# Kernel tuning notes

Hardware: AMD Instinct MI355X
Metric: run time of the kernel (lower is better)

## Reference

```python
import jax, jax.numpy as jnp
import numpy as np

N = 50000
HEADS1, HIM = 8, 16
NEG_SLOPE = 0.2


def gat_conv(x, src, dst, W, a_src, a_dst, bias, heads, out_dim, concat):
    n = x.shape[0]
    h = (x @ W).reshape(n, heads, out_dim)                      # [N,H,D]
    al_src = jnp.einsum('nhd,hd->nh', h, a_src)                  # [N,H]
    al_dst = jnp.einsum('nhd,hd->nh', h, a_dst)                  # [N,H]
    e = jax.nn.leaky_relu(al_src[src] + al_dst[dst], NEG_SLOPE)  # [E,H]
    # segment softmax over incoming edges of each destination node
    e_max = jax.ops.segment_max(e, dst, num_segments=n)
    e_max = jnp.where(jnp.isfinite(e_max), e_max, 0.0)
    ex = jnp.exp(e - e_max[dst])
    denom = jax.ops.segment_sum(ex, dst, num_segments=n)
    denom = jnp.where(denom == 0.0, 1.0, denom)
    alpha = ex / denom[dst]                                      # [E,H]
    msg = h[src] * alpha[:, :, None]                             # [E,H,D]
    out = jax.ops.segment_sum(msg, dst, num_segments=n)          # [N,H,D]
    out = out.reshape(n, heads * out_dim) if concat else out.mean(axis=1)
    return out + bias


def setup_inputs() -> dict:
    key = jax.random.key(0)
    ks = jax.random.split(key, 12)
    num_feature, out_feature, him = 128, 121, HIM
    E = 800000
    x = jax.random.normal(ks[0], (N, num_feature), dtype=jnp.float32)
    edge_index = jax.random.randint(ks[1], (2, E), 0, N, dtype=jnp.int64)
    s = 0.1
    W1 = jax.random.normal(ks[2], (num_feature, HEADS1 * him), dtype=jnp.float32) * s
    a_src1 = jax.random.normal(ks[3], (HEADS1, him), dtype=jnp.float32) * s
    a_dst1 = jax.random.normal(ks[4], (HEADS1, him), dtype=jnp.float32) * s
    b1 = jnp.zeros((HEADS1 * him,), dtype=jnp.float32)
    W2 = jax.random.normal(ks[5], (HEADS1 * him, out_feature), dtype=jnp.float32) * s
    a_src2 = jax.random.normal(ks[6], (1, out_feature), dtype=jnp.float32) * s
    a_dst2 = jax.random.normal(ks[7], (1, out_feature), dtype=jnp.float32) * s
    b2 = jnp.zeros((out_feature,), dtype=jnp.float32)
    return {"x": x, "edge_index": edge_index, "W1": W1, "a_src1": a_src1,
            "a_dst1": a_dst1, "b1": b1, "W2": W2, "a_src2": a_src2,
            "a_dst2": a_dst2, "b2": b2}


def reference(x, edge_index, W1, a_src1, a_dst1, b1, W2, a_src2, a_dst2, b2):
    n = x.shape[0]
    loops = jnp.arange(n, dtype=edge_index.dtype)
    src = jnp.concatenate([edge_index[0], loops])  # add self-loops (PyG default)
    dst = jnp.concatenate([edge_index[1], loops])
    h = gat_conv(x, src, dst, W1, a_src1, a_dst1, b1, HEADS1, HIM, True)
    h = jax.nn.relu(h)
    out = gat_conv(h, src, dst, W2, a_src2, a_dst2, b2, 1, W2.shape[1], True)
    return out
```

## Files before the change

kernel.cpp:

```cpp
#include <hip/hip_runtime.h>
#include <hip/hip_fp16.h>

#define NEG_SLOPE 0.2f

typedef __fp16 half8v __attribute__((ext_vector_type(8)));
typedef float f32x4 __attribute__((ext_vector_type(4)));
typedef unsigned uint4u __attribute__((ext_vector_type(4), aligned(4)));
typedef float f32x4u __attribute__((ext_vector_type(4), aligned(4)));

__device__ __forceinline__ float lrelu(float x) {
    return fmaxf(x, 0.0f) + NEG_SLOPE * fminf(x, 0.0f);
}

__device__ __forceinline__ unsigned fkey(float f) {
    unsigned u = __float_as_uint(f);
    return (u & 0x80000000u) ? ~u : (u | 0x80000000u);
}
__device__ __forceinline__ float funkey(unsigned k) {
    return __uint_as_float((k & 0x80000000u) ? (k & 0x7fffffffu) : ~k);
}


__global__ __launch_bounds__(256) void scan_reduce(const int* __restrict__ cnt,
                                                   int* __restrict__ bsum, int n) {
    __shared__ int sm[256];
    int base = blockIdx.x * 1024 + threadIdx.x * 4;
    int s = 0;
#pragma unroll
    for (int j = 0; j < 4; ++j) {
        int i = base + j;
        if (i < n) s += cnt[i];
    }
    sm[threadIdx.x] = s;
    __syncthreads();
#pragma unroll
    for (int off = 128; off >= 1; off >>= 1) {
        if (threadIdx.x < off) sm[threadIdx.x] += sm[threadIdx.x + off];
        __syncthreads();
    }
    if (threadIdx.x == 0) bsum[blockIdx.x] = sm[0];
}

__global__ __launch_bounds__(256) void scan_bsum256(int* __restrict__ bsum, int nb) {
    __shared__ int sm[256];
    int v = (threadIdx.x < (unsigned)nb) ? bsum[threadIdx.x] : 0;
    sm[threadIdx.x] = v;
    __syncthreads();
    for (int off = 1; off < 256; off <<= 1) {
        int y = (threadIdx.x >= off) ? sm[threadIdx.x - off] : 0;
        __syncthreads();
        sm[threadIdx.x] += y;
        __syncthreads();
    }
    if (threadIdx.x < (unsigned)nb) bsum[threadIdx.x] = sm[threadIdx.x] - v;
}

__global__ __launch_bounds__(256) void scan_write(const int* __restrict__ cnt,
                                                  const int* __restrict__ bsum,
                                                  int* __restrict__ rp, int n) {
    __shared__ int sm[256];
    int base = blockIdx.x * 1024 + threadIdx.x * 4;
    int v[4];
    int s = 0;
#pragma unroll
    for (int j = 0; j < 4; ++j) {
        int i = base + j;
        v[j] = (i < n) ? cnt[i] : 0;
        s += v[j];
    }
    sm[threadIdx.x] = s;
    __syncthreads();
#pragma unroll
    for (int off = 1; off < 256; off <<= 1) {
        int y = (threadIdx.x >= off) ? sm[threadIdx.x - off] : 0;
        __syncthreads();
        sm[threadIdx.x] += y;
        __syncthreads();
    }
    int run = sm[threadIdx.x] - s + bsum[blockIdx.x];
#pragma unroll
    for (int j = 0; j < 4; ++j) {
        int i = base + j;
        if (i < n) {
            rp[i] = run;
            run += v[j];
            if (i == n - 1) rp[n] = run;
        }
    }
}


__global__ __launch_bounds__(256) void rhist1_kernel(const int* __restrict__ dst,
                                                     int* __restrict__ h, int E, int nblk) {
    __shared__ int lh[256];
    lh[threadIdx.x] = 0;
    __syncthreads();
    int base = blockIdx.x * 1024;
#pragma unroll
    for (int j = 0; j < 4; ++j) {
        int i = base + j * 256 + threadIdx.x;
        if (i < E) atomicAdd(&lh[dst[i] & 255], 1);
    }
    __syncthreads();
    h[threadIdx.x * nblk + blockIdx.x] = lh[threadIdx.x];
}

__global__ __launch_bounds__(256) void rhist2_kernel(const unsigned* __restrict__ kv,
                                                     int* __restrict__ h, int E, int nblk) {
    __shared__ int lh[256];
    lh[threadIdx.x] = 0;
    __syncthreads();
    int base = blockIdx.x * 1024;
#pragma unroll
    for (int j = 0; j < 4; ++j) {
        int i = base + j * 256 + threadIdx.x;
        if (i < E) atomicAdd(&lh[kv[i] >> 24], 1);
    }
    __syncthreads();
    h[threadIdx.x * nblk + blockIdx.x] = lh[threadIdx.x];
}

template <int SH, bool PACK>
__global__ __launch_bounds__(256) void rscat_kernel(const unsigned* __restrict__ in,
                                                    const int* __restrict__ srcp,
                                                    const int* __restrict__ dstp,
                                                    unsigned* __restrict__ outv,
                                                    const int* __restrict__ scanned,
                                                    int E, int nblk) {
    __shared__ unsigned items[1024];
    __shared__ unsigned sorted[1024];
    __shared__ int lh[256], lstart[256], rbase[256];
    __shared__ int wcnt[4][256];

    int tid = threadIdx.x, blk = blockIdx.x;
    int base = blk * 1024;
    int k = min(1024, E - base);
    lh[tid] = 0;
    rbase[tid] = 0;
#pragma unroll
    for (int j = 0; j < 4; ++j) {
        int idx = j * 256 + tid;
        unsigned v = 0u;
        if (base + idx < E) {
            if constexpr (PACK)
                v = ((unsigned)dstp[base + idx] << 16) | (unsigned)srcp[base + idx];
            else
                v = in[base + idx];
        }
        items[idx] = v;
    }
    __syncthreads();
#pragma unroll
    for (int j = 0; j < 4; ++j) {
        int idx = j * 256 + tid;
        if (idx < k) atomicAdd(&lh[(items[idx] >> SH) & 255], 1);
    }
    __syncthreads();
    int sv = lh[tid];
    lstart[tid] = sv;
    __syncthreads();
    for (int off = 1; off < 256; off <<= 1) {
        int y = (tid >= off) ? lstart[tid - off] : 0;
        __syncthreads();
        lstart[tid] += y;
        __syncthreads();
    }
    int excl = lstart[tid] - sv;
    __syncthreads();
    lstart[tid] = excl;
    __syncthreads();

    int lane = tid & 63, wave = tid >> 6;
#pragma unroll
    for (int it = 0; it < 4; ++it) {
        int idx = it * 256 + tid;
        unsigned v = items[idx];
        int d = (v >> SH) & 255;
        bool valid = idx < k;
        unsigned long long m = __ballot(valid);
#pragma unroll
        for (int b = 0; b < 8; ++b) {
            unsigned long long bb = __ballot((d >> b) & 1);
            m &= ((d >> b) & 1) ? bb : ~bb;
        }
        int lanerank = __popcll(m & ((1ull << lane) - 1ull));
        int wtot = __popcll(m);
        wcnt[0][tid] = 0; wcnt[1][tid] = 0; wcnt[2][tid] = 0; wcnt[3][tid] = 0;
        __syncthreads();
        if (valid && lanerank == 0) wcnt[wave][d] = wtot;
        __syncthreads();
        if (valid) {
            int cw = 0;
            for (int w = 0; w < wave; ++w) cw += wcnt[w][d];
            sorted[lstart[d] + rbase[d] + cw + lanerank] = v;
        }
        __syncthreads();
        rbase[tid] += wcnt[0][tid] + wcnt[1][tid] + wcnt[2][tid] + wcnt[3][tid];
        __syncthreads();
    }
#pragma unroll
    for (int j = 0; j < 4; ++j) {
        int i = j * 256 + tid;
        if (i < k) {
            unsigned v = sorted[i];
            int d = (v >> SH) & 255;
            outv[scanned[d * nblk + blk] + (i - lstart[d])] = v;
        }
    }
}


__global__ void rp_kernel(const unsigned* __restrict__ kv, int* __restrict__ rp,
                          int E, int N) {
    int i = blockIdx.x * 256 + threadIdx.x;
    if (i >= E) return;
    int cur = (int)(kv[i] >> 16);
    int prev = (i == 0) ? -1 : (int)(kv[i - 1] >> 16);
    for (int t = prev + 1; t <= cur; ++t) rp[t] = i;
    if (i == E - 1)
        for (int t = cur + 1; t <= N; ++t) rp[t] = E;
}


template <int H>
__global__ __launch_bounds__(256) void gmax_kernel(const float* __restrict__ a,
                                                   unsigned* __restrict__ gm, int total) {
    __shared__ unsigned sm[256];
    unsigned loc = 0;
    int stride = 256 * gridDim.x;
    for (int i = blockIdx.x * 256 + threadIdx.x; i < total; i += stride)
        loc = max(loc, fkey(a[i]));
    sm[threadIdx.x] = loc;
    __syncthreads();
    for (int off = 128; off >= H; off >>= 1) {
        if (threadIdx.x < off) sm[threadIdx.x] = max(sm[threadIdx.x], sm[threadIdx.x + off]);
        __syncthreads();
    }
    if (threadIdx.x < H) atomicMax(&gm[threadIdx.x], sm[threadIdx.x]);
}


__global__ __launch_bounds__(256) void w1_kernel(const unsigned* __restrict__ kv,
                                                 const float* __restrict__ alS,
                                                 const float* __restrict__ alD,
                                                 const unsigned* __restrict__ gm,
                                                 float* __restrict__ w1t, int E) {
    int e = blockIdx.x * 256 + threadIdx.x;
    if (e >= E) return;
    unsigned k = kv[e];
    int s = (int)(k & 0xFFFFu), t = (int)(k >> 16);
    float sv[8], dv[8];
    *(f32x4*)&sv[0] = *(const f32x4*)(alS + (size_t)s * 8);
    *(f32x4*)&sv[4] = *(const f32x4*)(alS + (size_t)s * 8 + 4);
    *(f32x4*)&dv[0] = *(const f32x4*)(alD + (size_t)t * 8);
    *(f32x4*)&dv[4] = *(const f32x4*)(alD + (size_t)t * 8 + 4);
#pragma unroll
    for (int h = 0; h < 8; ++h) {
        float m = lrelu(funkey(gm[h]) + dv[h]);
        w1t[(size_t)h * E + e] = __expf(lrelu(sv[h] + dv[h]) - m);
    }
}

__global__ void w2_kernel(const unsigned* __restrict__ kv, const float* __restrict__ alS,
                          const float* __restrict__ alD, const unsigned* __restrict__ gm,
                          float* __restrict__ w2v, int E) {
    int e = blockIdx.x * 256 + threadIdx.x;
    if (e >= E) return;
    unsigned k = kv[e];
    int s = (int)(k & 0xFFFFu), t = (int)(k >> 16);
    float adT = alD[t];
    w2v[e] = __expf(lrelu(alS[s] + adT) - lrelu(funkey(gm[0]) + adT));
}


template <int NC, typename AT>
__global__ __launch_bounds__(256) void gemm_mfma(const AT* __restrict__ A,
                                                 const float* __restrict__ B,
                                                 __half* __restrict__ C, int M) {
    __shared__ __half Bt[128][136];

    {
        int t = threadIdx.x;
        int c = t & 127;
        int kq = t >> 7;
#pragma unroll
        for (int ch = 0; ch < 8; ++ch) {
            int k0 = kq * 64 + ch * 8;
            half8v hv;
#pragma unroll
            for (int j = 0; j < 8; ++j) {
                float v = (c < NC) ? B[(size_t)(k0 + j) * NC + c] : 0.0f;
                hv[j] = (__fp16)v;
            }
            *(half8v*)&Bt[c][k0] = hv;
        }
    }
    __syncthreads();

    const int wid = threadIdx.x >> 6;
    const int lane = threadIdx.x & 63;
    const int li = lane & 15;
    const int lg = lane >> 4;

    int row = blockIdx.x * 64 + wid * 16 + li;
    int rowc = min(row, M - 1);

    half8v a[4];
#pragma unroll
    for (int ks = 0; ks < 4; ++ks) {
        int q = ks * 4 + lg;
        if constexpr (sizeof(AT) == 2) {
            a[ks] = *((const half8v*)(A + (size_t)rowc * 128) + q);
        } else {
            const float4* p = (const float4*)(A + (size_t)rowc * 128) + 2 * q;
            float4 a0 = p[0], a1 = p[1];
            half8v hv;
            hv[0] = (__fp16)a0.x; hv[1] = (__fp16)a0.y; hv[2] = (__fp16)a0.z; hv[3] = (__fp16)a0.w;
            hv[4] = (__fp16)a1.x; hv[5] = (__fp16)a1.y; hv[6] = (__fp16)a1.z; hv[7] = (__fp16)a1.w;
            a[ks] = hv;
        }
    }

    f32x4 acc[8];
#pragma unroll
    for (int ct = 0; ct < 8; ++ct) acc[ct] = (f32x4)0.0f;

#pragma unroll
    for (int ks = 0; ks < 4; ++ks) {
#pragma unroll
        for (int ct = 0; ct < 8; ++ct) {
            half8v b = *(const half8v*)&Bt[ct * 16 + li][ks * 32 + 8 * lg];
            acc[ct] = __builtin_amdgcn_mfma_f32_16x16x32_f16(a[ks], b, acc[ct], 0, 0, 0);
        }
    }

    int orow = blockIdx.x * 64 + wid * 16 + 4 * lg;
#pragma unroll
    for (int ct = 0; ct < 8; ++ct) {
#pragma unroll
        for (int r = 0; r < 4; ++r) {
            int rr = orow + r;
            if (rr < M) C[(size_t)rr * 128 + ct * 16 + li] = __float2half(acc[ct][r]);
        }
    }
}


__global__ void al1_kernel(const __half* __restrict__ h1h, const float* __restrict__ as,
                           const float* __restrict__ ad, float* __restrict__ alS,
                           float* __restrict__ alD, int N) {
    int g = blockIdx.x * 256 + threadIdx.x;
    if (g >= N * 8) return;
    int r = g >> 3, h = g & 7;
    const __half2* hp = (const __half2*)(h1h + (size_t)r * 128 + h * 16);
    const float* sp = as + h * 16;
    const float* dp = ad + h * 16;
    float s = 0.f, d = 0.f;
#pragma unroll
    for (int q = 0; q < 8; ++q) {
        float2 v = __half22float2(hp[q]);
        s = fmaf(v.x, sp[2 * q], s);
        d = fmaf(v.x, dp[2 * q], d);
        s = fmaf(v.y, sp[2 * q + 1], s);
        d = fmaf(v.y, dp[2 * q + 1], d);
    }
    alS[g] = s;
    alD[g] = d;
}

__global__ __launch_bounds__(256) void al2_kernel(const __half* __restrict__ h3h,
                                                  const float* __restrict__ as,
                                                  const float* __restrict__ ad,
                                                  float* __restrict__ alS,
                                                  float* __restrict__ alD, int N, int NC) {
    int lane = threadIdx.x & 63;
    int r = blockIdx.x * 4 + (threadIdx.x >> 6);
    if (r >= N) return;
    float s = 0.f, d = 0.f;
    for (int c = lane; c < NC; c += 64) {
        float v = __half2float(h3h[(size_t)r * 128 + c]);
        s = fmaf(v, as[c], s);
        d = fmaf(v, ad[c], d);
    }
#pragma unroll
    for (int off = 32; off; off >>= 1) {
        s += __shfl_down(s, off);
        d += __shfl_down(d, off);
    }
    if (lane == 0) { alS[r] = s; alD[r] = d; }
}


__global__ __launch_bounds__(256) void agg1_kernel(
    const __half* __restrict__ h1h, const float* __restrict__ alS,
    const float* __restrict__ alD, const float* __restrict__ b1,
    const int* __restrict__ rp, const unsigned* __restrict__ kv,
    const float* __restrict__ w1t, const unsigned* __restrict__ gm,
    __half* __restrict__ h2h, int N, int E) {
    int t = blockIdx.x * 4 + (threadIdx.x >> 6);
    int lane = threadIdx.x & 63;
    int h = lane >> 3;

    float adh = alD[t * 8 + h];
    float mh = lrelu(funkey(gm[h]) + adh);
    int e0 = rp[t], e1 = rp[t + 1];

    float ex = __expf(lrelu(alS[t * 8 + h] + adh) - mh);
    float dsum = ex, dsum2 = 0.f;
    float2 hs = __half22float2(*(const __half2*)(h1h + (size_t)t * 128 + 2 * lane));
    float fx = ex * hs.x, fy = ex * hs.y;
    const float* wrow = w1t + (size_t)h * E;

    int e = e0;
    for (; e + 16 <= e1; e += 16) {
        uint4u kk[4];
        f32x4u ww[4];
#pragma unroll
        for (int q = 0; q < 4; ++q) {
            kk[q] = *(const uint4u*)&kv[e + 4 * q];
            ww[q] = *(const f32x4u*)&wrow[e + 4 * q];
        }
        float2 ff[16];
#pragma unroll
        for (int q = 0; q < 4; ++q)
#pragma unroll
            for (int r = 0; r < 4; ++r)
                ff[q * 4 + r] = __half22float2(
                    *(const __half2*)(h1h + (size_t)(kk[q][r] & 0xFFFFu) * 128 + 2 * lane));
#pragma unroll
        for (int q = 0; q < 4; ++q) {
            if (q & 1) dsum2 += (ww[q][0] + ww[q][1]) + (ww[q][2] + ww[q][3]);
            else       dsum  += (ww[q][0] + ww[q][1]) + (ww[q][2] + ww[q][3]);
#pragma unroll
            for (int r = 0; r < 4; ++r) {
                float w = ww[q][r];
                float2 f = ff[q * 4 + r];
                fx = fmaf(w, f.x, fx);
                fy = fmaf(w, f.y, fy);
            }
        }
    }
    if (e + 8 <= e1) {
        uint4u ka = *(const uint4u*)&kv[e];
        uint4u kb = *(const uint4u*)&kv[e + 4];
        f32x4u wa = *(const f32x4u*)&wrow[e];
        f32x4u wb = *(const f32x4u*)&wrow[e + 4];
        float2 f0 = __half22float2(*(const __half2*)(h1h + (size_t)(ka.x & 0xFFFFu) * 128 + 2 * lane));
        float2 f1 = __half22float2(*(const __half2*)(h1h + (size_t)(ka.y & 0xFFFFu) * 128 + 2 * lane));
        float2 f2 = __half22float2(*(const __half2*)(h1h + (size_t)(ka.z & 0xFFFFu) * 128 + 2 * lane));
        float2 f3 = __half22float2(*(const __half2*)(h1h + (size_t)(ka.w & 0xFFFFu) * 128 + 2 * lane));
        float2 f4 = __half22float2(*(const __half2*)(h1h + (size_t)(kb.x & 0xFFFFu) * 128 + 2 * lane));
        float2 f5 = __half22float2(*(const __half2*)(h1h + (size_t)(kb.y & 0xFFFFu) * 128 + 2 * lane));
        float2 f6 = __half22float2(*(const __half2*)(h1h + (size_t)(kb.z & 0xFFFFu) * 128 + 2 * lane));
        float2 f7 = __half22float2(*(const __half2*)(h1h + (size_t)(kb.w & 0xFFFFu) * 128 + 2 * lane));
        dsum += (wa[0] + wa[1]) + (wa[2] + wa[3]);
        dsum2 += (wb[0] + wb[1]) + (wb[2] + wb[3]);
        fx = fmaf(wa[0], f0.x, fx); fy = fmaf(wa[0], f0.y, fy);
        fx = fmaf(wa[1], f1.x, fx); fy = fmaf(wa[1], f1.y, fy);
        fx = fmaf(wa[2], f2.x, fx); fy = fmaf(wa[2], f2.y, fy);
        fx = fmaf(wa[3], f3.x, fx); fy = fmaf(wa[3], f3.y, fy);
        fx = fmaf(wb[0], f4.x, fx); fy = fmaf(wb[0], f4.y, fy);
        fx = fmaf(wb[1], f5.x, fx); fy = fmaf(wb[1], f5.y, fy);
        fx = fmaf(wb[2], f6.x, fx); fy = fmaf(wb[2], f6.y, fy);
        fx = fmaf(wb[3], f7.x, fx); fy = fmaf(wb[3], f7.y, fy);
        e += 8;
    }
    if (e + 4 <= e1) {
        uint4u ka = *(const uint4u*)&kv[e];
        f32x4u wa = *(const f32x4u*)&wrow[e];
        float2 f0 = __half22float2(*(const __half2*)(h1h + (size_t)(ka.x & 0xFFFFu) * 128 + 2 * lane));
        float2 f1 = __half22float2(*(const __half2*)(h1h + (size_t)(ka.y & 0xFFFFu) * 128 + 2 * lane));
        float2 f2 = __half22float2(*(const __half2*)(h1h + (size_t)(ka.z & 0xFFFFu) * 128 + 2 * lane));
        float2 f3 = __half22float2(*(const __half2*)(h1h + (size_t)(ka.w & 0xFFFFu) * 128 + 2 * lane));
        dsum += (wa[0] + wa[1]) + (wa[2] + wa[3]);
        fx = fmaf(wa[0], f0.x, fx); fy = fmaf(wa[0], f0.y, fy);
        fx = fmaf(wa[1], f1.x, fx); fy = fmaf(wa[1], f1.y, fy);
        fx = fmaf(wa[2], f2.x, fx); fy = fmaf(wa[2], f2.y, fy);
        fx = fmaf(wa[3], f3.x, fx); fy = fmaf(wa[3], f3.y, fy);
        e += 4;
    }
    for (; e < e1; ++e) {
        int s0 = (int)(kv[e] & 0xFFFFu);
        float w0 = wrow[e];
        float2 f0 = __half22float2(*(const __half2*)(h1h + (size_t)s0 * 128 + 2 * lane));
        dsum2 += w0;
        fx = fmaf(w0, f0.x, fx); fy = fmaf(w0, f0.y, fy);
    }
    dsum += dsum2;
    float inv = 1.0f / dsum;
    float2 bb = *(const float2*)(b1 + 2 * lane);
    float ox = fmaxf(fmaf(fx, inv, bb.x), 0.0f);
    float oy = fmaxf(fmaf(fy, inv, bb.y), 0.0f);
    *(__half2*)(h2h + (size_t)t * 128 + 2 * lane) = __floats2half2_rn(ox, oy);
}


__global__ __launch_bounds__(256) void agg2_kernel(
    const __half* __restrict__ h3h, const float* __restrict__ alS,
    const float* __restrict__ alD, const float* __restrict__ b2,
    const int* __restrict__ rp, const unsigned* __restrict__ kv,
    const float* __restrict__ w2v, const unsigned* __restrict__ gm,
    float* __restrict__ out, int N, int NC) {
    int t = blockIdx.x * 4 + (threadIdx.x >> 6);
    int lane = threadIdx.x & 63;

    float adT = alD[t];
    float m = lrelu(funkey(gm[0]) + adT);
    int e0 = rp[t], e1 = rp[t + 1];

    float ex = __expf(lrelu(alS[t] + adT) - m);
    float dsum = ex, dsum2 = 0.f;
    float2 hs = __half22float2(*(const __half2*)(h3h + (size_t)t * 128 + 2 * lane));
    float fx = ex * hs.x, fy = ex * hs.y;

    int e = e0;
    for (; e + 16 <= e1; e += 16) {
        uint4u kk[4];
        f32x4u ww[4];
#pragma unroll
        for (int q = 0; q < 4; ++q) {
            kk[q] = *(const uint4u*)&kv[e + 4 * q];
            ww[q] = *(const f32x4u*)&w2v[e + 4 * q];
        }
        float2 ff[16];
#pragma unroll
        for (int q = 0; q < 4; ++q)
#pragma unroll
            for (int r = 0; r < 4; ++r)
                ff[q * 4 + r] = __half22float2(
                    *(const __half2*)(h3h + (size_t)(kk[q][r] & 0xFFFFu) * 128 + 2 * lane));
#pragma unroll
        for (int q = 0; q < 4; ++q) {
            if (q & 1) dsum2 += (ww[q][0] + ww[q][1]) + (ww[q][2] + ww[q][3]);
            else       dsum  += (ww[q][0] + ww[q][1]) + (ww[q][2] + ww[q][3]);
#pragma unroll
            for (int r = 0; r < 4; ++r) {
                float w = ww[q][r];
                float2 f = ff[q * 4 + r];
                fx = fmaf(w, f.x, fx);
                fy = fmaf(w, f.y, fy);
            }
        }
    }
    if (e + 8 <= e1) {
        uint4u ka = *(const uint4u*)&kv[e];
        uint4u kb = *(const uint4u*)&kv[e + 4];
        f32x4u wa = *(const f32x4u*)&w2v[e];
        f32x4u wb = *(const f32x4u*)&w2v[e + 4];
        float2 f0 = __half22float2(*(const __half2*)(h3h + (size_t)(ka.x & 0xFFFFu) * 128 + 2 * lane));
        float2 f1 = __half22float2(*(const __half2*)(h3h + (size_t)(ka.y & 0xFFFFu) * 128 + 2 * lane));
        float2 f2 = __half22float2(*(const __half2*)(h3h + (size_t)(ka.z & 0xFFFFu) * 128 + 2 * lane));
        float2 f3 = __half22float2(*(const __half2*)(h3h + (size_t)(ka.w & 0xFFFFu) * 128 + 2 * lane));
        float2 f4 = __half22float2(*(const __half2*)(h3h + (size_t)(kb.x & 0xFFFFu) * 128 + 2 * lane));
        float2 f5 = __half22float2(*(const __half2*)(h3h + (size_t)(kb.y & 0xFFFFu) * 128 + 2 * lane));
        float2 f6 = __half22float2(*(const __half2*)(h3h + (size_t)(kb.z & 0xFFFFu) * 128 + 2 * lane));
        float2 f7 = __half22float2(*(const __half2*)(h3h + (size_t)(kb.w & 0xFFFFu) * 128 + 2 * lane));
        dsum += (wa[0] + wa[1]) + (wa[2] + wa[3]);
        dsum2 += (wb[0] + wb[1]) + (wb[2] + wb[3]);
        fx = fmaf(wa[0], f0.x, fx); fy = fmaf(wa[0], f0.y, fy);
        fx = fmaf(wa[1], f1.x, fx); fy = fmaf(wa[1], f1.y, fy);
        fx = fmaf(wa[2], f2.x, fx); fy = fmaf(wa[2], f2.y, fy);
        fx = fmaf(wa[3], f3.x, fx); fy = fmaf(wa[3], f3.y, fy);
        fx = fmaf(wb[0], f4.x, fx); fy = fmaf(wb[0], f4.y, fy);
        fx = fmaf(wb[1], f5.x, fx); fy = fmaf(wb[1], f5.y, fy);
        fx = fmaf(wb[2], f6.x, fx); fy = fmaf(wb[2], f6.y, fy);
        fx = fmaf(wb[3], f7.x, fx); fy = fmaf(wb[3], f7.y, fy);
        e += 8;
    }
    if (e + 4 <= e1) {
        uint4u ka = *(const uint4u*)&kv[e];
        f32x4u wa = *(const f32x4u*)&w2v[e];
        float2 f0 = __half22float2(*(const __half2*)(h3h + (size_t)(ka.x & 0xFFFFu) * 128 + 2 * lane));
        float2 f1 = __half22float2(*(const __half2*)(h3h + (size_t)(ka.y & 0xFFFFu) * 128 + 2 * lane));
        float2 f2 = __half22float2(*(const __half2*)(h3h + (size_t)(ka.z & 0xFFFFu) * 128 + 2 * lane));
        float2 f3 = __half22float2(*(const __half2*)(h3h + (size_t)(ka.w & 0xFFFFu) * 128 + 2 * lane));
        dsum += (wa[0] + wa[1]) + (wa[2] + wa[3]);
        fx = fmaf(wa[0], f0.x, fx); fy = fmaf(wa[0], f0.y, fy);
        fx = fmaf(wa[1], f1.x, fx); fy = fmaf(wa[1], f1.y, fy);
        fx = fmaf(wa[2], f2.x, fx); fy = fmaf(wa[2], f2.y, fy);
        fx = fmaf(wa[3], f3.x, fx); fy = fmaf(wa[3], f3.y, fy);
        e += 4;
    }
    for (; e < e1; ++e) {
        int s0 = (int)(kv[e] & 0xFFFFu);
        float w0 = w2v[e];
        float2 f0 = __half22float2(*(const __half2*)(h3h + (size_t)s0 * 128 + 2 * lane));
        dsum2 += w0;
        fx = fmaf(w0, f0.x, fx); fy = fmaf(w0, f0.y, fy);
    }
    dsum += dsum2;
    float inv = 1.0f / dsum;
    int c0 = 2 * lane, c1 = 2 * lane + 1;
    if (c0 < NC) out[(size_t)t * NC + c0] = fmaf(fx, inv, b2[c0]);
    if (c1 < NC) out[(size_t)t * NC + c1] = fmaf(fy, inv, b2[c1]);
}


extern "C" void kernel_launch(void* const* d_in, const int* in_sizes, int n_in,
                              void* d_out, int out_size, void* d_ws, size_t ws_size,
                              hipStream_t stream) {
    const float* x   = (const float*)d_in[0];
    const int*   ei  = (const int*)d_in[1];
    const float* W1  = (const float*)d_in[2];
    const float* aS1 = (const float*)d_in[3];
    const float* aD1 = (const float*)d_in[4];
    const float* b1  = (const float*)d_in[5];
    const float* W2  = (const float*)d_in[6];
    const float* aS2 = (const float*)d_in[7];
    const float* aD2 = (const float*)d_in[8];
    const float* b2  = (const float*)d_in[9];
    float* out = (float*)d_out;

    const int N = in_sizes[0] / 128;
    const int E = in_sizes[1] / 2;
    const int NC2 = 121;

    const int NBLK = (E + 1023) / 1024;
    const int HN = 256 * NBLK;

    size_t off = 0;
    auto alloc = [&](size_t bytes) {
        size_t o = off;
        off = (off + bytes + 255) & ~(size_t)255;
        return o;
    };
    char* ws = (char*)d_ws;
    unsigned* kv0  = (unsigned*)(ws + alloc((size_t)E * 4));
    unsigned* kv1  = (unsigned*)(ws + alloc((size_t)E * 4));
    int*      h    = (int*)(ws + alloc((size_t)(HN + 1) * 4));
    int*      hs   = (int*)(ws + alloc((size_t)(HN + 1) * 4));
    int*      rp   = (int*)(ws + alloc((size_t)(N + 1) * 4));
    int*      bsum = (int*)(ws + alloc(256 * 4));
    float*    alS1 = (float*)(ws + alloc((size_t)N * 8 * 4));
    float*    alD1 = (float*)(ws + alloc((size_t)N * 8 * 4));
    float*    alS2 = (float*)(ws + alloc((size_t)N * 4));
    float*    alD2 = (float*)(ws + alloc((size_t)N * 4));
    unsigned* gm1  = (unsigned*)(ws + alloc(8 * 4));
    unsigned* gm2  = (unsigned*)(ws + alloc(4));
    float*    w1t  = (float*)(ws + alloc((size_t)E * 8 * 4));
    __half*   h1h  = (__half*)(ws + alloc((size_t)N * 128 * 2));
    __half*   h2h  = (__half*)(ws + alloc((size_t)N * 128 * 2));
    __half*   h3h  = h1h;
    float*    w2v  = (float*)kv1;
    if (ws_size < off) return;

    const int* src = ei;
    const int* dst = ei + E;

    hipMemsetAsync(gm1, 0, 8 * 4, stream);
    hipMemsetAsync(gm2, 0, 4, stream);

    int eb = (E + 255) / 256;
    int snb = (HN + 1023) / 1024;

    rhist1_kernel<<<NBLK, 256, 0, stream>>>(dst, h, E, NBLK);
    scan_reduce<<<snb, 256, 0, stream>>>(h, bsum, HN);
    scan_bsum256<<<1, 256, 0, stream>>>(bsum, snb);
    scan_write<<<snb, 256, 0, stream>>>(h, bsum, hs, HN);
    rscat_kernel<16, true><<<NBLK, 256, 0, stream>>>(nullptr, src, dst, kv1, hs, E, NBLK);
    rhist2_kernel<<<NBLK, 256, 0, stream>>>(kv1, h, E, NBLK);
    scan_reduce<<<snb, 256, 0, stream>>>(h, bsum, HN);
    scan_bsum256<<<1, 256, 0, stream>>>(bsum, snb);
    scan_write<<<snb, 256, 0, stream>>>(h, bsum, hs, HN);
    rscat_kernel<24, false><<<NBLK, 256, 0, stream>>>(kv1, nullptr, nullptr, kv0, hs, E, NBLK);
    rp_kernel<<<eb, 256, 0, stream>>>(kv0, rp, E, N);

    int gmb = (N + 63) / 64;
    int ab = (N + 3) / 4;
    gemm_mfma<128, float><<<gmb, 256, 0, stream>>>(x, W1, h1h, N);
    al1_kernel<<<(N * 8 + 255) / 256, 256, 0, stream>>>(h1h, aS1, aD1, alS1, alD1, N);
    gmax_kernel<8><<<128, 256, 0, stream>>>(alS1, gm1, N * 8);
    w1_kernel<<<eb, 256, 0, stream>>>(kv0, alS1, alD1, gm1, w1t, E);
    agg1_kernel<<<ab, 256, 0, stream>>>(h1h, alS1, alD1, b1, rp, kv0, w1t, gm1, h2h, N, E);

    gemm_mfma<121, __half><<<gmb, 256, 0, stream>>>(h2h, W2, h3h, N);
    al2_kernel<<<ab, 256, 0, stream>>>(h3h, aS2, aD2, alS2, alD2, N, NC2);
    gmax_kernel<1><<<128, 256, 0, stream>>>(alS2, gm2, N);
    w2_kernel<<<eb, 256, 0, stream>>>(kv0, alS2, alD2, gm2, w2v, E);
    agg2_kernel<<<ab, 256, 0, stream>>>(h3h, alS2, alD2, b2, rp, kv0, w2v, gm2, out, N, NC2);
}
```

Measured before the change: 209.5 us.

## Store layer-1 edge weights in fp16 and fuse layer-2 attention logits into GEMM

Layer-1 per-edge exponentiated weights are now stored as fp16 instead of fp32, which halves the w1t write and read traffic between w1_kernel and agg1_kernel. agg1 gains a scalar prologue that aligns the edge index to a multiple of 4 so the half4 vector loads stay aligned. The separate al2_kernel is removed: the layer-2 GEMM computes the source and destination attention dot products from its fp32 accumulators using a shuffle reduction across lanes. In exchange, the edge weights lose precision, and the layer-2 logits are now computed from unrounded fp32 values rather than from the fp16 output.

```diff
diff --git a/kernel.cpp b/kernel.cpp
--- a/kernel.cpp
+++ b/kernel.cpp
@@ -4,6 +4,7 @@
 #define NEG_SLOPE 0.2f
 
 typedef __fp16 half8v __attribute__((ext_vector_type(8)));
+typedef __fp16 half4v __attribute__((ext_vector_type(4)));
 typedef float f32x4 __attribute__((ext_vector_type(4)));
 typedef unsigned uint4u __attribute__((ext_vector_type(4), aligned(4)));
 typedef float f32x4u __attribute__((ext_vector_type(4), aligned(4)));
@@ -244,7 +245,7 @@
                                                  const float* __restrict__ alS,
                                                  const float* __restrict__ alD,
                                                  const unsigned* __restrict__ gm,
-                                                 float* __restrict__ w1t, int E) {
+                                                 __half* __restrict__ w1t, int E) {
     int e = blockIdx.x * 256 + threadIdx.x;
     if (e >= E) return;
     unsigned k = kv[e];
@@ -257,7 +258,7 @@
 #pragma unroll
     for (int h = 0; h < 8; ++h) {
         float m = lrelu(funkey(gm[h]) + dv[h]);
-        w1t[(size_t)h * E + e] = __expf(lrelu(sv[h] + dv[h]) - m);
+        w1t[(size_t)h * E + e] = __float2half(__expf(lrelu(sv[h] + dv[h]) - m));
     }
 }
 
@@ -273,10 +274,14 @@
 }
 
 
-template <int NC, typename AT>
+template <int NC, typename AT, bool FUSE_AL2>
 __global__ __launch_bounds__(256) void gemm_mfma(const AT* __restrict__ A,
                                                  const float* __restrict__ B,
-                                                 __half* __restrict__ C, int M) {
+                                                 __half* __restrict__ C, int M,
+                                                 const float* __restrict__ as,
+                                                 const float* __restrict__ ad,
+                                                 float* __restrict__ alS,
+                                                 float* __restrict__ alD) {
     __shared__ __half Bt[128][136];
 
     {
@@ -343,6 +348,33 @@
             if (rr < M) C[(size_t)rr * 128 + ct * 16 + li] = __float2half(acc[ct][r]);
         }
     }
+
+    if constexpr (FUSE_AL2) {
+        float asv[8], adv[8];
+#pragma unroll
+        for (int ct = 0; ct < 8; ++ct) {
+            int c = ct * 16 + li;
+            asv[ct] = (c < NC) ? as[c] : 0.0f;
+            adv[ct] = (c < NC) ? ad[c] : 0.0f;
+        }
+#pragma unroll
+        for (int r = 0; r < 4; ++r) {
+            float s = 0.f, d = 0.f;
+#pragma unroll
+            for (int ct = 0; ct < 8; ++ct) {
+                s = fmaf(acc[ct][r], asv[ct], s);
+                d = fmaf(acc[ct][r], adv[ct], d);
+            }
+            s += __shfl_down(s, 8); d += __shfl_down(d, 8);
+            s += __shfl_down(s, 4); d += __shfl_down(d, 4);
+            s += __shfl_down(s, 2); d += __shfl_down(d, 2);
+            s += __shfl_down(s, 1); d += __shfl_down(d, 1);
+            if (li == 0) {
+                int rr = orow + r;
+                if (rr < M) { alS[rr] = s; alD[rr] = d; }
+            }
+        }
+    }
 }
 
 
@@ -368,34 +400,12 @@
     alD[g] = d;
 }
 
-__global__ __launch_bounds__(256) void al2_kernel(const __half* __restrict__ h3h,
-                                                  const float* __restrict__ as,
-                                                  const float* __restrict__ ad,
-                                                  float* __restrict__ alS,
-                                                  float* __restrict__ alD, int N, int NC) {
-    int lane = threadIdx.x & 63;
-    int r = blockIdx.x * 4 + (threadIdx.x >> 6);
-    if (r >= N) return;
-    float s = 0.f, d = 0.f;
-    for (int c = lane; c < NC; c += 64) {
-        float v = __half2float(h3h[(size_t)r * 128 + c]);
-        s = fmaf(v, as[c], s);
-        d = fmaf(v, ad[c], d);
-    }
-#pragma unroll
-    for (int off = 32; off; off >>= 1) {
-        s += __shfl_down(s, off);
-        d += __shfl_down(d, off);
-    }
-    if (lane == 0) { alS[r] = s; alD[r] = d; }
-}
-
 
 __global__ __launch_bounds__(256) void agg1_kernel(
     const __half* __restrict__ h1h, const float* __restrict__ alS,
     const float* __restrict__ alD, const float* __restrict__ b1,
     const int* __restrict__ rp, const unsigned* __restrict__ kv,
-    const float* __restrict__ w1t, const unsigned* __restrict__ gm,
+    const __half* __restrict__ w1t, const unsigned* __restrict__ gm,
     __half* __restrict__ h2h, int N, int E) {
     int t = blockIdx.x * 4 + (threadIdx.x >> 6);
     int lane = threadIdx.x & 63;
@@ -409,16 +419,26 @@
     float dsum = ex, dsum2 = 0.f;
     float2 hs = __half22float2(*(const __half2*)(h1h + (size_t)t * 128 + 2 * lane));
     float fx = ex * hs.x, fy = ex * hs.y;
-    const float* wrow = w1t + (size_t)h * E;
+    const __half* wrow = w1t + (size_t)h * E;
 
     int e = e0;
+    while (e < e1 && (e & 3)) {
+        int s0 = (int)(kv[e] & 0xFFFFu);
+        float w0 = __half2float(wrow[e]);
+        float2 f0 = __half22float2(*(const __half2*)(h1h + (size_t)s0 * 128 + 2 * lane));
+        dsum2 += w0;
+        fx = fmaf(w0, f0.x, fx); fy = fmaf(w0, f0.y, fy);
+        ++e;
+    }
     for (; e + 16 <= e1; e += 16) {
         uint4u kk[4];
-        f32x4u ww[4];
+        float ww[16];
 #pragma unroll
         for (int q = 0; q < 4; ++q) {
             kk[q] = *(const uint4u*)&kv[e + 4 * q];
-            ww[q] = *(const f32x4u*)&wrow[e + 4 * q];
+            half4v wv = *(const half4v*)&wrow[e + 4 * q];
+#pragma unroll
+            for (int r = 0; r < 4; ++r) ww[q * 4 + r] = (float)wv[r];
         }
         float2 ff[16];
 #pragma unroll
@@ -429,11 +449,11 @@
                     *(const __half2*)(h1h + (size_t)(kk[q][r] & 0xFFFFu) * 128 + 2 * lane));
 #pragma unroll
         for (int q = 0; q < 4; ++q) {
-            if (q & 1) dsum2 += (ww[q][0] + ww[q][1]) + (ww[q][2] + ww[q][3]);
-            else       dsum  += (ww[q][0] + ww[q][1]) + (ww[q][2] + ww[q][3]);
+            if (q & 1) dsum2 += (ww[q * 4] + ww[q * 4 + 1]) + (ww[q * 4 + 2] + ww[q * 4 + 3]);
+            else       dsum  += (ww[q * 4] + ww[q * 4 + 1]) + (ww[q * 4 + 2] + ww[q * 4 + 3]);
 #pragma unroll
             for (int r = 0; r < 4; ++r) {
-                float w = ww[q][r];
+                float w = ww[q * 4 + r];
                 float2 f = ff[q * 4 + r];
                 fx = fmaf(w, f.x, fx);
                 fy = fmaf(w, f.y, fy);
@@ -443,8 +463,8 @@
     if (e + 8 <= e1) {
         uint4u ka = *(const uint4u*)&kv[e];
         uint4u kb = *(const uint4u*)&kv[e + 4];
-        f32x4u wa = *(const f32x4u*)&wrow[e];
-        f32x4u wb = *(const f32x4u*)&wrow[e + 4];
+        half4v wva = *(const half4v*)&wrow[e];
+        half4v wvb = *(const half4v*)&wrow[e + 4];
         float2 f0 = __half22float2(*(const __half2*)(h1h + (size_t)(ka.x & 0xFFFFu) * 128 + 2 * lane));
         float2 f1 = __half22float2(*(const __half2*)(h1h + (size_t)(ka.y & 0xFFFFu) * 128 + 2 * lane));
         float2 f2 = __half22float2(*(const __half2*)(h1h + (size_t)(ka.z & 0xFFFFu) * 128 + 2 * lane));
@@ -453,35 +473,38 @@
         float2 f5 = __half22float2(*(const __half2*)(h1h + (size_t)(kb.y & 0xFFFFu) * 128 + 2 * lane));
         float2 f6 = __half22float2(*(const __half2*)(h1h + (size_t)(kb.z & 0xFFFFu) * 128 + 2 * lane));
         float2 f7 = __half22float2(*(const __half2*)(h1h + (size_t)(kb.w & 0xFFFFu) * 128 + 2 * lane));
-        dsum += (wa[0] + wa[1]) + (wa[2] + wa[3]);
-        dsum2 += (wb[0] + wb[1]) + (wb[2] + wb[3]);
-        fx = fmaf(wa[0], f0.x, fx); fy = fmaf(wa[0], f0.y, fy);
-        fx = fmaf(wa[1], f1.x, fx); fy = fmaf(wa[1], f1.y, fy);
-        fx = fmaf(wa[2], f2.x, fx); fy = fmaf(wa[2], f2.y, fy);
-        fx = fmaf(wa[3], f3.x, fx); fy = fmaf(wa[3], f3.y, fy);
-        fx = fmaf(wb[0], f4.x, fx); fy = fmaf(wb[0], f4.y, fy);
-        fx = fmaf(wb[1], f5.x, fx); fy = fmaf(wb[1], f5.y, fy);
-        fx = fmaf(wb[2], f6.x, fx); fy = fmaf(wb[2], f6.y, fy);
-        fx = fmaf(wb[3], f7.x, fx); fy = fmaf(wb[3], f7.y, fy);
+        float w0 = (float)wva[0], w1 = (float)wva[1], w2 = (float)wva[2], w3 = (float)wva[3];
+        float w4 = (float)wvb[0], w5 = (float)wvb[1], w6 = (float)wvb[2], w7 = (float)wvb[3];
+        dsum += (w0 + w1) + (w2 + w3);
+        dsum2 += (w4 + w5) + (w6 + w7);
+        fx = fmaf(w0, f0.x, fx); fy = fmaf(w0, f0.y, fy);
+        fx = fmaf(w1, f1.x, fx); fy = fmaf(w1, f1.y, fy);
+        fx = fmaf(w2, f2.x, fx); fy = fmaf(w2, f2.y, fy);
+        fx = fmaf(w3, f3.x, fx); fy = fmaf(w3, f3.y, fy);
+        fx = fmaf(w4, f4.x, fx); fy = fmaf(w4, f4.y, fy);
+        fx = fmaf(w5, f5.x, fx); fy = fmaf(w5, f5.y, fy);
+        fx = fmaf(w6, f6.x, fx); fy = fmaf(w6, f6.y, fy);
+        fx = fmaf(w7, f7.x, fx); fy = fmaf(w7, f7.y, fy);
         e += 8;
     }
     if (e + 4 <= e1) {
         uint4u ka = *(const uint4u*)&kv[e];
-        f32x4u wa = *(const f32x4u*)&wrow[e];
+        half4v wva = *(const half4v*)&wrow[e];
         float2 f0 = __half22float2(*(const __half2*)(h1h + (size_t)(ka.x & 0xFFFFu) * 128 + 2 * lane));
         float2 f1 = __half22float2(*(const __half2*)(h1h + (size_t)(ka.y & 0xFFFFu) * 128 + 2 * lane));
         float2 f2 = __half22float2(*(const __half2*)(h1h + (size_t)(ka.z & 0xFFFFu) * 128 + 2 * lane));
         float2 f3 = __half22float2(*(const __half2*)(h1h + (size_t)(ka.w & 0xFFFFu) * 128 + 2 * lane));
-        dsum += (wa[0] + wa[1]) + (wa[2] + wa[3]);
-        fx = fmaf(wa[0], f0.x, fx); fy = fmaf(wa[0], f0.y, fy);
-        fx = fmaf(wa[1], f1.x, fx); fy = fmaf(wa[1], f1.y, fy);
-        fx = fmaf(wa[2], f2.x, fx); fy = fmaf(wa[2], f2.y, fy);
-        fx = fmaf(wa[3], f3.x, fx); fy = fmaf(wa[3], f3.y, fy);
+        float w0 = (float)wva[0], w1 = (float)wva[1], w2 = (float)wva[2], w3 = (float)wva[3];
+        dsum += (w0 + w1) + (w2 + w3);
+        fx = fmaf(w0, f0.x, fx); fy = fmaf(w0, f0.y, fy);
+        fx = fmaf(w1, f1.x, fx); fy = fmaf(w1, f1.y, fy);
+        fx = fmaf(w2, f2.x, fx); fy = fmaf(w2, f2.y, fy);
+        fx = fmaf(w3, f3.x, fx); fy = fmaf(w3, f3.y, fy);
         e += 4;
     }
     for (; e < e1; ++e) {
         int s0 = (int)(kv[e] & 0xFFFFu);
-        float w0 = wrow[e];
+        float w0 = __half2float(wrow[e]);
         float2 f0 = __half22float2(*(const __half2*)(h1h + (size_t)s0 * 128 + 2 * lane));
         dsum2 += w0;
         fx = fmaf(w0, f0.x, fx); fy = fmaf(w0, f0.y, fy);
@@ -637,7 +660,7 @@
     float*    alD2 = (float*)(ws + alloc((size_t)N * 4));
     unsigned* gm1  = (unsigned*)(ws + alloc(8 * 4));
     unsigned* gm2  = (unsigned*)(ws + alloc(4));
-    float*    w1t  = (float*)(ws + alloc((size_t)E * 8 * 4));
+    __half*   w1t  = (__half*)(ws + alloc((size_t)E * 8 * 2));
     __half*   h1h  = (__half*)(ws + alloc((size_t)N * 128 * 2));
     __half*   h2h  = (__half*)(ws + alloc((size_t)N * 128 * 2));
     __half*   h3h  = h1h;
@@ -667,14 +690,15 @@
 
     int gmb = (N + 63) / 64;
     int ab = (N + 3) / 4;
-    gemm_mfma<128, float><<<gmb, 256, 0, stream>>>(x, W1, h1h, N);
+    gemm_mfma<128, float, false><<<gmb, 256, 0, stream>>>(x, W1, h1h, N,
+                                                          nullptr, nullptr, nullptr, nullptr);
     al1_kernel<<<(N * 8 + 255) / 256, 256, 0, stream>>>(h1h, aS1, aD1, alS1, alD1, N);
     gmax_kernel<8><<<128, 256, 0, stream>>>(alS1, gm1, N * 8);
     w1_kernel<<<eb, 256, 0, stream>>>(kv0, alS1, alD1, gm1, w1t, E);
     agg1_kernel<<<ab, 256, 0, stream>>>(h1h, alS1, alD1, b1, rp, kv0, w1t, gm1, h2h, N, E);
 
-    gemm_mfma<121, __half><<<gmb, 256, 0, stream>>>(h2h, W2, h3h, N);
-    al2_kernel<<<ab, 256, 0, stream>>>(h3h, aS2, aD2, alS2, alD2, N, NC2);
+    gemm_mfma<121, __half, true><<<gmb, 256, 0, stream>>>(h2h, W2, h3h, N,
+                                                          aS2, aD2, alS2, alD2);
     gmax_kernel<1><<<128, 256, 0, stream>>>(alS2, gm2, N);
     w2_kernel<<<eb, 256, 0, stream>>>(kv0, alS2, alD2, gm2, w2v, E);
     agg2_kernel<<<ab, 256, 0, stream>>>(h3h, alS2, alD2, b2, rp, kv0, w2v, gm2, out, N, NC2);
```

Result: faster. 200.8 us (-4.1%).
